# Kernel tuning notes

Hardware: AMD Instinct MI355X
Metric: run time of the kernel (lower is better)

Reference implementation:

```python
import jax, jax.numpy as jnp
import numpy as np

EMBED = 1024
HEADS = 16
DK = EMBED // HEADS


def setup_inputs() -> dict:
    key = jax.random.key(0)
    ks = jax.random.split(key, 6)
    B, S = 2, 2048
    scale = 1.0 / np.sqrt(EMBED)
    x = jax.random.normal(ks[0], (B, S, EMBED), dtype=jnp.float32)
    Wq = jax.random.normal(ks[1], (EMBED, EMBED), dtype=jnp.float32) * scale
    Wk = jax.random.normal(ks[2], (EMBED, EMBED), dtype=jnp.float32) * scale
    Wv = jax.random.normal(ks[3], (EMBED, EMBED), dtype=jnp.float32) * scale
    Wo = jax.random.normal(ks[4], (EMBED, EMBED), dtype=jnp.float32) * scale
    qw = jnp.zeros((HEADS, 1), dtype=jnp.float32)  # quantum_weight, init quantum_scale=0
    return {"x": x, "Wq": Wq, "Wk": Wk, "Wv": Wv, "Wo": Wo, "qw": qw}


def reference(x, Wq, Wk, Wv, Wo, qw):
    B, S, E = x.shape
    # nn.Linear with no bias: y = x @ W.T; split heads -> [B,H,S,Dk]
    def proj(W):
        return (x @ W.T).reshape(B, S, HEADS, DK).transpose(0, 2, 1, 3)
    q, k, v = proj(Wq), proj(Wk), proj(Wv)
    scores = jnp.einsum('bhsd,bhtd->bhst', q, k) / np.sqrt(DK)
    attn = jax.nn.softmax(scores, axis=-1)  # dropout in eval mode: identity
    classical = jnp.einsum('bhst,bhtd->bhsd', attn, v)
    w = jax.nn.sigmoid(qw)[:, :, None]  # [H,1,1] per-head mixing weight
    out = w * jnp.sin(classical) + (1.0 - w) * classical
    out = out.transpose(0, 2, 1, 3).reshape(B, S, E)
    return out @ Wo.T
```

## Files before the change

kernel.cpp:

```cpp
#include <hip/hip_runtime.h>
#include <math.h>

constexpr int Ec  = 1024;
constexpr int Hc  = 16;
constexpr int DKc = 64;
constexpr int Bc  = 2;
constexpr int Sc  = 2048;
constexpr int Mc  = Bc * Sc;

typedef _Float16 half8 __attribute__((ext_vector_type(8)));
typedef _Float16 half4 __attribute__((ext_vector_type(4)));
typedef float    floatx4  __attribute__((ext_vector_type(4)));
typedef float    floatx16 __attribute__((ext_vector_type(16)));
typedef unsigned int uint2v __attribute__((ext_vector_type(2)));
typedef unsigned int uint4v __attribute__((ext_vector_type(4)));

#define MFMA16(a, b, c) __builtin_amdgcn_mfma_f32_16x16x32_f16(a, b, c, 0, 0, 0)
#define MFMA32(a, b, c) __builtin_amdgcn_mfma_f32_32x32x16_f16(a, b, c, 0, 0, 0)

__device__ __forceinline__ void async_lds16(const _Float16* g, _Float16* l)
{
    __builtin_amdgcn_global_load_lds(
        (const __attribute__((address_space(1))) unsigned int*)g,
        (__attribute__((address_space(3))) unsigned int*)l, 16, 0, 0);
}

__device__ __forceinline__ unsigned pkh2(float a, float b)
{
    return __builtin_bit_cast(unsigned, __builtin_amdgcn_cvt_pkrtz(a, b));
}

__global__ __launch_bounds__(256)
void convert_to_h(const float4* __restrict__ x,
                  const float4* __restrict__ wq,
                  const float4* __restrict__ wk,
                  const float4* __restrict__ wv,
                  const float4* __restrict__ wo,
                  half4* __restrict__ dst)
{
    const int i = blockIdx.x * 256 + threadIdx.x;
    const float4* src; int off;
    if      (i < 1048576) { src = x;  off = i; }
    else if (i < 1310720) { src = wq; off = i - 1048576; }
    else if (i < 1572864) { src = wk; off = i - 1310720; }
    else if (i < 1835008) { src = wv; off = i - 1572864; }
    else                  { src = wo; off = i - 1835008; }
    const float4 v = src[off];
    half4 o;
    o.x = (_Float16)v.x; o.y = (_Float16)v.y;
    o.z = (_Float16)v.z; o.w = (_Float16)v.w;
    dst[i] = o;
}

__device__ __forceinline__ void mfma_gemm_core64(const _Float16* __restrict__ A,
                                                 const _Float16* __restrict__ Bw,
                                                 int m0, int n0,
                                                 _Float16* As, _Float16* Bs,
                                                 floatx4 acc[4][4])
{
    const int tid  = threadIdx.x;
    const int wave = tid >> 6, lane = tid & 63;
    const int l16  = lane & 15, quad = lane >> 4;
    const int wrow = (wave >> 1) * 64, wcol = (wave & 1) * 64;

    const int srow8  = lane >> 3;
    const int schunk = (lane & 7) ^ (srow8 & 7);
    const _Float16* ga = A  + (size_t)(m0 + wave * 32 + srow8) * Ec + schunk * 8;
    const _Float16* gb = Bw + (size_t)(n0 + wave * 32 + srow8) * Ec + schunk * 8;
    _Float16* lA = As + (size_t)(wave * 32) * 64;
    _Float16* lB = Bs + (size_t)(wave * 32) * 64;

    for (int kt = 0; kt < Ec; kt += 64) {
#pragma unroll
        for (int c = 0; c < 4; ++c) {
            async_lds16(ga + (size_t)(c * 8) * Ec + kt, lA + c * 512);
            async_lds16(gb + (size_t)(c * 8) * Ec + kt, lB + c * 512);
        }
        __syncthreads();

        half8 af[4][2], bf[4][2];
#pragma unroll
        for (int i = 0; i < 4; ++i) {
            const int ra = wrow + i * 16 + l16;
            const int rb = wcol + i * 16 + l16;
#pragma unroll
            for (int kc = 0; kc < 2; ++kc) {
                af[i][kc] = *(const half8*)&As[ra * 64 + (((quad + kc * 4) ^ (ra & 7)) * 8)];
                bf[i][kc] = *(const half8*)&Bs[rb * 64 + (((quad + kc * 4) ^ (rb & 7)) * 8)];
            }
        }
#pragma unroll
        for (int i = 0; i < 4; ++i)
#pragma unroll
            for (int j = 0; j < 4; ++j) {
                acc[i][j] = MFMA16(af[i][0], bf[j][0], acc[i][j]);
                acc[i][j] = MFMA16(af[i][1], bf[j][1], acc[i][j]);
            }
        __syncthreads();
    }
}

__global__ __launch_bounds__(256)
void gemm_qkv_fused(const _Float16* __restrict__ xh,
                    const _Float16* __restrict__ wall,
                    _Float16* __restrict__ Qh,
                    _Float16* __restrict__ Kh,
                    _Float16* __restrict__ VTh)
{
    __shared__ __align__(16) _Float16 As[128 * 64];
    __shared__ __align__(16) _Float16 Bs[128 * 64];
    const int lin = blockIdx.x;
    const int swz = (lin & 7) * 96 + (lin >> 3);
    const int m0  = (swz / 24) * 128;
    const int n0f = (swz % 24) * 128;

    floatx4 acc[4][4] = {};
    mfma_gemm_core64(xh, wall, m0, n0f, As, Bs, acc);

    const int tid  = threadIdx.x;
    const int wave = tid >> 6, lane = tid & 63;
    const int l16  = lane & 15, quad = lane >> 4;
    const int wrow = (wave >> 1) * 64, wcol = (wave & 1) * 64;

    const int z   = n0f >> 10;
    const int nl0 = n0f & 1023;

    if (z == 2) {
#pragma unroll
        for (int i = 0; i < 4; ++i)
#pragma unroll
            for (int j = 0; j < 4; ++j) {
                const int n  = nl0 + wcol + j * 16 + l16;
                const int hh = n >> 6, d = n & 63;
                const int mb = m0 + wrow + i * 16 + quad * 4;
                const int bb = mb >> 11, s = mb & (Sc - 1);
                half4 pk;
#pragma unroll
                for (int r = 0; r < 4; ++r) pk[r] = (_Float16)acc[i][j][r];
                *(half4*)&VTh[((size_t)((bb * Hc + hh) * DKc + d)) * Sc + s] = pk;
            }
    } else {
        _Float16* out = (z == 0) ? Qh : Kh;
        const float scale = (z == 0) ? 0.18033688011112042f : 1.0f;
#pragma unroll
        for (int i = 0; i < 4; ++i)
#pragma unroll
            for (int j = 0; j < 4; ++j) {
                const int n = nl0 + wcol + j * 16 + l16;
#pragma unroll
                for (int r = 0; r < 4; ++r) {
                    const int m = m0 + wrow + i * 16 + quad * 4 + r;
                    out[(size_t)m * Ec + n] = (_Float16)(acc[i][j][r] * scale);
                }
            }
    }
}

__global__ __launch_bounds__(256)
void gemm_out_mfma(const _Float16* __restrict__ A,
                   const _Float16* __restrict__ W,
                   float* __restrict__ C)
{
    __shared__ __align__(16) _Float16 As[128 * 64];
    __shared__ __align__(16) _Float16 Bs[64 * 64];
    const int lin = blockIdx.x;
    const int swz = (lin & 7) * 64 + (lin >> 3);
    const int m0 = (swz >> 4) * 128, n0 = (swz & 15) * 64;

    const int tid  = threadIdx.x;
    const int wave = tid >> 6, lane = tid & 63;
    const int l16  = lane & 15, quad = lane >> 4;
    const int wrow = (wave >> 1) * 64, wcol = (wave & 1) * 32;

    const int srow8  = lane >> 3;
    const int schunk = (lane & 7) ^ (srow8 & 7);
    const _Float16* ga = A + (size_t)(m0 + wave * 32 + srow8) * Ec + schunk * 8;
    const _Float16* gb = W + (size_t)(n0 + wave * 16 + srow8) * Ec + schunk * 8;
    _Float16* lA = As + (size_t)(wave * 32) * 64;
    _Float16* lB = Bs + (size_t)(wave * 16) * 64;

    floatx4 acc[4][2] = {};

    for (int kt = 0; kt < Ec; kt += 64) {
#pragma unroll
        for (int c = 0; c < 4; ++c)
            async_lds16(ga + (size_t)(c * 8) * Ec + kt, lA + c * 512);
#pragma unroll
        for (int c = 0; c < 2; ++c)
            async_lds16(gb + (size_t)(c * 8) * Ec + kt, lB + c * 512);
        __syncthreads();

        half8 af[4][2], bf[2][2];
#pragma unroll
        for (int i = 0; i < 4; ++i) {
            const int ra = wrow + i * 16 + l16;
#pragma unroll
            for (int kc = 0; kc < 2; ++kc)
                af[i][kc] = *(const half8*)&As[ra * 64 + (((quad + kc * 4) ^ (ra & 7)) * 8)];
        }
#pragma unroll
        for (int j = 0; j < 2; ++j) {
            const int rb = wcol + j * 16 + l16;
#pragma unroll
            for (int kc = 0; kc < 2; ++kc)
                bf[j][kc] = *(const half8*)&Bs[rb * 64 + (((quad + kc * 4) ^ (rb & 7)) * 8)];
        }
#pragma unroll
        for (int i = 0; i < 4; ++i)
#pragma unroll
            for (int j = 0; j < 2; ++j) {
                acc[i][j] = MFMA16(af[i][0], bf[j][0], acc[i][j]);
                acc[i][j] = MFMA16(af[i][1], bf[j][1], acc[i][j]);
            }
        __syncthreads();
    }

#pragma unroll
    for (int i = 0; i < 4; ++i)
#pragma unroll
        for (int j = 0; j < 2; ++j) {
            const int n = n0 + wcol + j * 16 + l16;
#pragma unroll
            for (int r = 0; r < 4; ++r) {
                const int m = m0 + wrow + i * 16 + quad * 4 + r;
                C[(size_t)m * Ec + n] = acc[i][j][r];
            }
        }
}

__global__ __launch_bounds__(512, 4)
void flash_attn(const _Float16* __restrict__ Qh,
                const _Float16* __restrict__ Kh,
                const _Float16* __restrict__ VTh,
                const float* __restrict__ qw,
                _Float16* __restrict__ Mixh)
{
    constexpr int BM = 128, BN = 64;
    constexpr int NT = (Sc / BN) / 2;
    __shared__ __align__(16) _Float16 KV[2][2][2][64 * 64];
    __shared__ float Ls[2][128];

    const int tid  = threadIdx.x;
    const int g    = tid >> 8;
    const int wl   = (tid >> 6) & 3;
    const int lane = tid & 63;
    const int l31  = lane & 31, hi = lane >> 5;
    const int q0 = blockIdx.x * BM;
    const int bh = blockIdx.y;
    const int h  = bh & (Hc - 1), b = bh >> 4;

    half8 aq[4];
    {
        const _Float16* qp = Qh + (size_t)(b * Sc + q0 + wl * 32 + l31) * Ec
                                + h * DKc + hi * 8;
#pragma unroll
        for (int ks = 0; ks < 4; ++ks) aq[ks] = *(const half8*)(qp + ks * 16);
    }

    const int srow   = lane >> 3;
    const int schunk = (lane & 7) ^ srow;
    const _Float16* Kg = Kh + (size_t)(b * Sc + g * (Sc / 2) + wl * 16 + srow) * Ec
                            + h * DKc + schunk * 8;
    const _Float16* Vg = VTh + ((size_t)(bh * DKc + wl * 16 + srow)) * Sc
                             + g * (Sc / 2) + schunk * 8;

    const int xk = l31 & 7;
    const _Float16* kbase[4];
    const _Float16* vbase[4];
#pragma unroll
    for (int ks = 0; ks < 4; ++ks) {
        const int xo = ((((ks << 1) | hi) ^ xk) << 3);
        kbase[ks] = KV[g][0][0] + l31 * 64 + xo;
        vbase[ks] = KV[g][0][1] + l31 * 64 + xo;
    }
    _Float16* kd0 = KV[g][0][0] + (wl * 16) * 64;
    _Float16* vd0 = KV[g][0][1] + (wl * 16) * 64;

    floatx16 o[2] = {};
    float l_run = 0.f;

    async_lds16(Kg, kd0);
    async_lds16(Kg + (size_t)8 * Ec, kd0 + 512);
    async_lds16(Vg, vd0);
    async_lds16(Vg + (size_t)8 * Sc, vd0 + 512);
    __syncthreads();

    const _Float16* kgp = Kg + (size_t)BN * Ec;
    const _Float16* vgp = Vg + BN;

#define ATTN_TILE(CO)                                                         \
    {                                                                         \
        _Pragma("unroll")                                                     \
        for (int t = 0; t < 2; ++t) {                                         \
            floatx16 st = {};                                                 \
            __builtin_amdgcn_s_setprio(1);                                    \
            _Pragma("unroll")                                                 \
            for (int ks = 0; ks < 4; ++ks)                                    \
                st = MFMA32(*(const half8*)(kbase[ks] + (CO) + t * 2048),     \
                            aq[ks], st);                                      \
            __builtin_amdgcn_s_setprio(0);                                    \
            float p[16];                                                      \
            _Pragma("unroll")                                                 \
            for (int r = 0; r < 16; ++r) p[r] = __builtin_amdgcn_exp2f(st[r]);\
            float s8[8];                                                      \
            _Pragma("unroll")                                                 \
            for (int r = 0; r < 8; ++r) s8[r] = p[2 * r] + p[2 * r + 1];      \
            float s4[4];                                                      \
            _Pragma("unroll")                                                 \
            for (int r = 0; r < 4; ++r) s4[r] = s8[2 * r] + s8[2 * r + 1];    \
            l_run += ((s4[0] + s4[1]) + (s4[2] + s4[3]));                     \
            half8 pa[2];                                                      \
            _Pragma("unroll")                                                 \
            for (int e = 0; e < 2; ++e) {                                     \
                const unsigned X0 = pkh2(p[8 * e + 0], p[8 * e + 1]);         \
                const unsigned X1 = pkh2(p[8 * e + 2], p[8 * e + 3]);         \
                const unsigned Y0 = pkh2(p[8 * e + 4], p[8 * e + 5]);         \
                const unsigned Y1 = pkh2(p[8 * e + 6], p[8 * e + 7]);         \
                const uint2v s0 = __builtin_amdgcn_permlane32_swap(X0, Y0, false, false); \
                const uint2v s1 = __builtin_amdgcn_permlane32_swap(X1, Y1, false, false); \
                uint4v w; w.x = s0.x; w.y = s1.x; w.z = s0.y; w.w = s1.y;     \
                pa[e] = __builtin_bit_cast(half8, w);                         \
            }                                                                 \
            __builtin_amdgcn_s_setprio(1);                                    \
            _Pragma("unroll")                                                 \
            for (int dt = 0; dt < 2; ++dt)                                    \
                _Pragma("unroll")                                             \
                for (int e = 0; e < 2; ++e) {                                 \
                    const half8 bv = *(const half8*)                          \
                        (vbase[2 * t + e] + (CO) + dt * 2048);                \
                    o[dt] = MFMA32(pa[e], bv, o[dt]);                         \
                }                                                             \
            __builtin_amdgcn_s_setprio(0);                                    \
        }                                                                     \
    }

    for (int n = 0; n < NT; n += 2) {
        async_lds16(kgp, kd0 + 8192);
        async_lds16(kgp + (size_t)8 * Ec, kd0 + 8192 + 512);
        async_lds16(vgp, vd0 + 8192);
        async_lds16(vgp + (size_t)8 * Sc, vd0 + 8192 + 512);
        kgp += (size_t)BN * Ec; vgp += BN;

        ATTN_TILE(0)
        __syncthreads();

        if (n + 2 < NT) {
            async_lds16(kgp, kd0);
            async_lds16(kgp + (size_t)8 * Ec, kd0 + 512);
            async_lds16(vgp, vd0);
            async_lds16(vgp + (size_t)8 * Sc, vd0 + 512);
            kgp += (size_t)BN * Ec; vgp += BN;
        }

        ATTN_TILE(8192)
        __syncthreads();
    }
#undef ATTN_TILE

    l_run += __shfl_xor(l_run, 32);
    if (hi == 0) Ls[g][wl * 32 + l31] = l_run;

    float* Os = (float*)&KV[0][0][0][0];
    if (g == 1) {
#pragma unroll
        for (int dt = 0; dt < 2; ++dt)
#pragma unroll
            for (int r = 0; r < 16; ++r) {
                const int row = wl * 32 + (r & 3) + 8 * (r >> 2) + 4 * hi;
                Os[row * 66 + dt * 32 + l31] = o[dt][r];
            }
    }
    __syncthreads();
    if (g == 0) {
        const float wmix = 1.f / (1.f + __expf(-qw[h]));
#pragma unroll
        for (int r = 0; r < 16; ++r) {
            const int row = wl * 32 + (r & 3) + 8 * (r >> 2) + 4 * hi;
            const float inv = 1.f / (Ls[0][row] + Ls[1][row]);
            _Float16* mp = Mixh + (size_t)(b * Sc + q0 + row) * Ec + h * DKc;
#pragma unroll
            for (int dt = 0; dt < 2; ++dt) {
                const float v = (o[dt][r] + Os[row * 66 + dt * 32 + l31]) * inv;
                mp[dt * 32 + l31] = (_Float16)(wmix * __sinf(v) + (1.f - wmix) * v);
            }
        }
    }
}

extern "C" void kernel_launch(void* const* d_in, const int* in_sizes, int n_in,
                              void* d_out, int out_size, void* d_ws, size_t ws_size,
                              hipStream_t stream)
{
    const float* x  = (const float*)d_in[0];
    const float* Wq = (const float*)d_in[1];
    const float* Wk = (const float*)d_in[2];
    const float* Wv = (const float*)d_in[3];
    const float* Wo = (const float*)d_in[4];
    const float* qw = (const float*)d_in[5];
    float* out = (float*)d_out;

    _Float16* hb   = (_Float16*)d_ws;
    _Float16* xh   = hb;
    _Float16* wqh  = hb + (size_t)4 * 1024 * 1024;
    _Float16* woh  = hb + (size_t)7 * 1024 * 1024;
    _Float16* Qh   = hb + (size_t)8 * 1024 * 1024;
    _Float16* Kh   = hb + (size_t)12 * 1024 * 1024;
    _Float16* VTh  = hb + (size_t)16 * 1024 * 1024;
    _Float16* mixh = hb + (size_t)20 * 1024 * 1024;

    convert_to_h<<<dim3(8192), dim3(256), 0, stream>>>(
        (const float4*)x, (const float4*)Wq, (const float4*)Wk,
        (const float4*)Wv, (const float4*)Wo, (half4*)hb);

    gemm_qkv_fused<<<dim3(768), dim3(256), 0, stream>>>(
        xh, wqh, Qh, Kh, VTh);

    flash_attn<<<dim3(Sc / 128, Bc * Hc), dim3(512), 0, stream>>>(
        Qh, Kh, VTh, qw, mixh);

    gemm_out_mfma<<<dim3(512), dim3(256), 0, stream>>>(
        mixh, woh, out);
}
```

Baseline: 189.7 us.

## Drop split-KV in flash attention, use 256-thread blocks with XCD-aware mapping

New measurement: 185.0 us. 2.5% less time.

```diff
diff --git a/kernel.cpp b/kernel.cpp
--- a/kernel.cpp
+++ b/kernel.cpp
@@ -228,7 +228,7 @@
         }
 }
 
-__global__ __launch_bounds__(512, 4)
+__global__ __launch_bounds__(256, 4)
 void flash_attn(const _Float16* __restrict__ Qh,
                 const _Float16* __restrict__ Kh,
                 const _Float16* __restrict__ VTh,
@@ -236,18 +236,20 @@
                 _Float16* __restrict__ Mixh)
 {
     constexpr int BM = 128, BN = 64;
-    constexpr int NT = (Sc / BN) / 2;
-    __shared__ __align__(16) _Float16 KV[2][2][2][64 * 64];
-    __shared__ float Ls[2][128];
+    constexpr int NT = Sc / BN;
+    __shared__ __align__(16) _Float16 KV[2][2][64 * 64];
 
     const int tid  = threadIdx.x;
-    const int g    = tid >> 8;
-    const int wl   = (tid >> 6) & 3;
+    const int wl   = tid >> 6;
     const int lane = tid & 63;
     const int l31  = lane & 31, hi = lane >> 5;
-    const int q0 = blockIdx.x * BM;
-    const int bh = blockIdx.y;
-    const int h  = bh & (Hc - 1), b = bh >> 4;
+
+    const int lin = blockIdx.x;
+    const int xcd = lin & 7, idx = lin >> 3;
+    const int bh  = xcd * 4 + (idx >> 4);
+    const int qx  = idx & 15;
+    const int q0  = qx * BM;
+    const int h   = bh & (Hc - 1), b = bh >> 4;
 
     half8 aq[4];
     {
@@ -259,10 +261,10 @@
 
     const int srow   = lane >> 3;
     const int schunk = (lane & 7) ^ srow;
-    const _Float16* Kg = Kh + (size_t)(b * Sc + g * (Sc / 2) + wl * 16 + srow) * Ec
+    const _Float16* Kg = Kh + (size_t)(b * Sc + wl * 16 + srow) * Ec
                             + h * DKc + schunk * 8;
     const _Float16* Vg = VTh + ((size_t)(bh * DKc + wl * 16 + srow)) * Sc
-                             + g * (Sc / 2) + schunk * 8;
+                             + schunk * 8;
 
     const int xk = l31 & 7;
     const _Float16* kbase[4];
@@ -270,11 +272,11 @@
 #pragma unroll
     for (int ks = 0; ks < 4; ++ks) {
         const int xo = ((((ks << 1) | hi) ^ xk) << 3);
-        kbase[ks] = KV[g][0][0] + l31 * 64 + xo;
-        vbase[ks] = KV[g][0][1] + l31 * 64 + xo;
-    }
-    _Float16* kd0 = KV[g][0][0] + (wl * 16) * 64;
-    _Float16* vd0 = KV[g][0][1] + (wl * 16) * 64;
+        kbase[ks] = KV[0][0] + l31 * 64 + xo;
+        vbase[ks] = KV[0][1] + l31 * 64 + xo;
+    }
+    _Float16* kd0 = KV[0][0] + (wl * 16) * 64;
+    _Float16* vd0 = KV[0][1] + (wl * 16) * 64;
 
     floatx16 o[2] = {};
     float l_run = 0.f;
@@ -293,12 +295,10 @@
         _Pragma("unroll")                                                     \
         for (int t = 0; t < 2; ++t) {                                         \
             floatx16 st = {};                                                 \
-            __builtin_amdgcn_s_setprio(1);                                    \
             _Pragma("unroll")                                                 \
             for (int ks = 0; ks < 4; ++ks)                                    \
                 st = MFMA32(*(const half8*)(kbase[ks] + (CO) + t * 2048),     \
                             aq[ks], st);                                      \
-            __builtin_amdgcn_s_setprio(0);                                    \
             float p[16];                                                      \
             _Pragma("unroll")                                                 \
             for (int r = 0; r < 16; ++r) p[r] = __builtin_amdgcn_exp2f(st[r]);\
@@ -321,7 +321,6 @@
                 uint4v w; w.x = s0.x; w.y = s1.x; w.z = s0.y; w.w = s1.y;     \
                 pa[e] = __builtin_bit_cast(half8, w);                         \
             }                                                                 \
-            __builtin_amdgcn_s_setprio(1);                                    \
             _Pragma("unroll")                                                 \
             for (int dt = 0; dt < 2; ++dt)                                    \
                 _Pragma("unroll")                                             \
@@ -330,7 +329,6 @@
                         (vbase[2 * t + e] + (CO) + dt * 2048);                \
                     o[dt] = MFMA32(pa[e], bv, o[dt]);                         \
                 }                                                             \
-            __builtin_amdgcn_s_setprio(0);                                    \
         }                                                                     \
     }
 
@@ -358,31 +356,17 @@
 #undef ATTN_TILE
 
     l_run += __shfl_xor(l_run, 32);
-    if (hi == 0) Ls[g][wl * 32 + l31] = l_run;
-
-    float* Os = (float*)&KV[0][0][0][0];
-    if (g == 1) {
-#pragma unroll
-        for (int dt = 0; dt < 2; ++dt)
-#pragma unroll
-            for (int r = 0; r < 16; ++r) {
-                const int row = wl * 32 + (r & 3) + 8 * (r >> 2) + 4 * hi;
-                Os[row * 66 + dt * 32 + l31] = o[dt][r];
-            }
-    }
-    __syncthreads();
-    if (g == 0) {
-        const float wmix = 1.f / (1.f + __expf(-qw[h]));
-#pragma unroll
-        for (int r = 0; r < 16; ++r) {
-            const int row = wl * 32 + (r & 3) + 8 * (r >> 2) + 4 * hi;
-            const float inv = 1.f / (Ls[0][row] + Ls[1][row]);
-            _Float16* mp = Mixh + (size_t)(b * Sc + q0 + row) * Ec + h * DKc;
-#pragma unroll
-            for (int dt = 0; dt < 2; ++dt) {
-                const float v = (o[dt][r] + Os[row * 66 + dt * 32 + l31]) * inv;
-                mp[dt * 32 + l31] = (_Float16)(wmix * __sinf(v) + (1.f - wmix) * v);
-            }
+
+    const float wmix = 1.f / (1.f + __expf(-qw[h]));
+#pragma unroll
+    for (int r = 0; r < 16; ++r) {
+        const int row = (r & 3) + 8 * (r >> 2) + 4 * hi;
+        const float inv = 1.f / __shfl(l_run, row);
+        _Float16* mp = Mixh + (size_t)(b * Sc + q0 + wl * 32 + row) * Ec + h * DKc;
+#pragma unroll
+        for (int dt = 0; dt < 2; ++dt) {
+            const float v = o[dt][r] * inv;
+            mp[dt * 32 + l31] = (_Float16)(wmix * __sinf(v) + (1.f - wmix) * v);
         }
     }
 }
@@ -415,7 +399,7 @@
     gemm_qkv_fused<<<dim3(768), dim3(256), 0, stream>>>(
         xh, wqh, Qh, Kh, VTh);
 
-    flash_attn<<<dim3(Sc / 128, Bc * Hc), dim3(512), 0, stream>>>(
+    flash_attn<<<dim3(512), dim3(256), 0, stream>>>(
         Qh, Kh, VTh, qw, mixh);
 
     gemm_out_mfma<<<dim3(512), dim3(256), 0, stream>>>(
```
